# Optimization experiments

Hardware: AMD Instinct MI355X
Metric: run time of the kernel (lower is better)

## Reference

```python
import jax, jax.numpy as jnp
import numpy as np

D = 512          # embedding_dim (cfg.hidden_size)
K = 1024         # codebook_size
DECAY = 0.99
EPS = 1e-05
COMMITMENT_COST = 0.25


def setup_inputs() -> dict:
    key = jax.random.key(0)
    k1, k2, k3 = jax.random.split(key, 3)
    return {
        "inputs": jax.random.normal(k1, (32, 1024, D), dtype=jnp.float32),
        "embedding_weight": jax.random.normal(k2, (K, D), dtype=jnp.float32),
        "ema_cluster_size": jnp.zeros((K,), dtype=jnp.float32),
        "ema_w": jax.random.normal(k3, (K, D), dtype=jnp.float32),
    }


def reference(inputs, embedding_weight, ema_cluster_size, ema_w):
    input_shape = inputs.shape
    flat = inputs.reshape(-1, D)  # [N, D]

    # Squared L2 distances to every codebook entry: [N, K]
    distances = (
        jnp.sum(flat ** 2, axis=1, keepdims=True)
        + jnp.sum(embedding_weight ** 2, axis=1)
        - 2.0 * flat @ embedding_weight.T
    )
    idx = jnp.argmin(distances, axis=1)                      # [N]
    encodings = jax.nn.one_hot(idx, K, dtype=flat.dtype)     # [N, K]

    # ---- EMA codebook update (training path) ----
    counts = jnp.sum(encodings, axis=0)                      # == bincount(idx)
    new_cs = ema_cluster_size * DECAY + (1.0 - DECAY) * counts
    n = jnp.sum(new_cs)
    new_cs = (new_cs + EPS) / (n + K * EPS) * n              # Laplace smoothing
    # dw = encodings.T @ flat, done as a fused gather-reduce instead of dense matmul
    dw = jax.ops.segment_sum(flat, idx, num_segments=K)      # [K, D]
    new_ema_w = ema_w * DECAY + (1.0 - DECAY) * dw
    new_embedding = new_ema_w / new_cs[:, None]              # updated codebook

    # quantized = encodings @ new_embedding, expressed as a gather
    quantized = new_embedding[idx].reshape(input_shape)

    e_latent_loss = jnp.mean((jax.lax.stop_gradient(quantized) - inputs) ** 2)
    loss = COMMITMENT_COST * e_latent_loss

    # straight-through estimator
    quantized = inputs + jax.lax.stop_gradient(quantized - inputs)

    avg_probs = jnp.mean(encodings, axis=0)
    perplexity = jnp.exp(-jnp.sum(avg_probs * jnp.log(avg_probs + 1e-10)))
    return (loss, quantized, perplexity, encodings)
```

## Files before the change

### kernel.cpp

```cpp
#include <hip/hip_runtime.h>

#define NROWS 32768
#define DIM   512
#define KC    1024

typedef __attribute__((ext_vector_type(8)))  short short8v;
typedef __attribute__((ext_vector_type(16))) float f32x16;

__global__ __launch_bounds__(256) void k_enorm(const float* __restrict__ E,
                                               float* __restrict__ en2) {
    int w = threadIdx.x >> 6, lane = threadIdx.x & 63;
    int c = blockIdx.x * 4 + w;
    const float* row = E + (size_t)c * DIM;
    float4 a = *reinterpret_cast<const float4*>(&row[lane * 8]);
    float4 b = *reinterpret_cast<const float4*>(&row[lane * 8 + 4]);
    float s = a.x*a.x + a.y*a.y + a.z*a.z + a.w*a.w
            + b.x*b.x + b.y*b.y + b.z*b.z + b.w*b.w;
    #pragma unroll
    for (int off = 32; off; off >>= 1) s += __shfl_xor(s, off);
    if (!lane) en2[c] = s;
}

__device__ __forceinline__ void split_bf16(float v, short& hi, short& lo) {
    unsigned u = __float_as_uint(v);
    unsigned r = u + 0x7FFFu + ((u >> 16) & 1u);
    hi = (short)(r >> 16);
    float hif = __uint_as_float(r & 0xFFFF0000u);
    float rem = v - hif;
    unsigned u2 = __float_as_uint(rem);
    unsigned r2 = u2 + 0x7FFFu + ((u2 >> 16) & 1u);
    lo = (short)(r2 >> 16);
}

__device__ __forceinline__ unsigned long long pack_key(float d, int c) {
    unsigned u = __float_as_uint(d);
    u = (u & 0x80000000u) ? ~u : (u | 0x80000000u);
    return ((unsigned long long)u << 32) | (unsigned)c;
}

__global__ __launch_bounds__(256, 2) void k_argmin(const float* __restrict__ x,
                                                   const float* __restrict__ E,
                                                   const float* __restrict__ en2,
                                                   unsigned long long* __restrict__ packed) {
    __shared__ short xhi[128][48], xlo[128][48];
    __shared__ short ehi[128][48], elo[128][48];
    const int tid = threadIdx.x;
    const int w = tid >> 6, l = tid & 63;
    const int wr = w >> 1, wc = w & 1;
    const int l31 = l & 31, lh = l >> 5;

    int bid = blockIdx.x;
    int xcd = bid & 7, j = bid >> 3;
    int row0 = (xcd * 32 + (j >> 3)) * 128;
    int c0   = (j & 7) * 128;

    f32x16 acc[2][2];
    #pragma unroll
    for (int a = 0; a < 2; ++a)
        #pragma unroll
        for (int b = 0; b < 2; ++b)
            #pragma unroll
            for (int r = 0; r < 16; ++r) acc[a][b][r] = 0.f;

    float4 rx[4], re[4];
    #pragma unroll
    for (int h = 0; h < 4; ++h) {
        int s = tid + h * 256, r = s >> 3, f4 = s & 7;
        rx[h] = *reinterpret_cast<const float4*>(&x[(size_t)(row0 + r) * DIM + f4 * 4]);
        re[h] = *reinterpret_cast<const float4*>(&E[(size_t)(c0   + r) * DIM + f4 * 4]);
    }

    for (int dt = 0; dt < DIM; dt += 32) {
        __syncthreads();
        #pragma unroll
        for (int h = 0; h < 4; ++h) {
            int s = tid + h * 256, r = s >> 3, f4 = s & 7;
            short4 h4, l4;
            split_bf16(rx[h].x, h4.x, l4.x); split_bf16(rx[h].y, h4.y, l4.y);
            split_bf16(rx[h].z, h4.z, l4.z); split_bf16(rx[h].w, h4.w, l4.w);
            *reinterpret_cast<short4*>(&xhi[r][f4 * 4]) = h4;
            *reinterpret_cast<short4*>(&xlo[r][f4 * 4]) = l4;
            split_bf16(re[h].x, h4.x, l4.x); split_bf16(re[h].y, h4.y, l4.y);
            split_bf16(re[h].z, h4.z, l4.z); split_bf16(re[h].w, h4.w, l4.w);
            *reinterpret_cast<short4*>(&ehi[r][f4 * 4]) = h4;
            *reinterpret_cast<short4*>(&elo[r][f4 * 4]) = l4;
        }
        __syncthreads();
        if (dt + 32 < DIM) {
            #pragma unroll
            for (int h = 0; h < 4; ++h) {
                int s = tid + h * 256, r = s >> 3, f4 = s & 7;
                rx[h] = *reinterpret_cast<const float4*>(
                    &x[(size_t)(row0 + r) * DIM + dt + 32 + f4 * 4]);
                re[h] = *reinterpret_cast<const float4*>(
                    &E[(size_t)(c0   + r) * DIM + dt + 32 + f4 * 4]);
            }
        }
        #pragma unroll
        for (int ks = 0; ks < 2; ++ks) {
            const int kb = ks * 16 + lh * 8;
            short8v axh[2], axl[2], beh[2], bel[2];
            #pragma unroll
            for (int tm = 0; tm < 2; ++tm) {
                int row = wr * 64 + tm * 32 + l31;
                axh[tm] = *reinterpret_cast<const short8v*>(&xhi[row][kb]);
                axl[tm] = *reinterpret_cast<const short8v*>(&xlo[row][kb]);
            }
            #pragma unroll
            for (int tn = 0; tn < 2; ++tn) {
                int col = wc * 64 + tn * 32 + l31;
                beh[tn] = *reinterpret_cast<const short8v*>(&ehi[col][kb]);
                bel[tn] = *reinterpret_cast<const short8v*>(&elo[col][kb]);
            }
            #pragma unroll
            for (int tm = 0; tm < 2; ++tm)
                #pragma unroll
                for (int tn = 0; tn < 2; ++tn) {
                    acc[tm][tn] = __builtin_amdgcn_mfma_f32_32x32x16_bf16(
                        axh[tm], beh[tn], acc[tm][tn], 0, 0, 0);
                    acc[tm][tn] = __builtin_amdgcn_mfma_f32_32x32x16_bf16(
                        axh[tm], bel[tn], acc[tm][tn], 0, 0, 0);
                    acc[tm][tn] = __builtin_amdgcn_mfma_f32_32x32x16_bf16(
                        axl[tm], beh[tn], acc[tm][tn], 0, 0, 0);
                }
        }
    }

    float e2[2];
    #pragma unroll
    for (int tn = 0; tn < 2; ++tn) e2[tn] = en2[c0 + wc * 64 + tn * 32 + l31];
    const int cA = c0 + wc * 64 + l31;
    #pragma unroll
    for (int tm = 0; tm < 2; ++tm) {
        #pragma unroll
        for (int r = 0; r < 16; ++r) {
            float d0 = fmaf(-2.f, acc[tm][0][r], e2[0]);
            float d1 = fmaf(-2.f, acc[tm][1][r], e2[1]);
            unsigned long long k0 = pack_key(d0, cA);
            unsigned long long k1 = pack_key(d1, cA + 32);
            unsigned long long key = k0 < k1 ? k0 : k1;
            #pragma unroll
            for (int off = 1; off < 32; off <<= 1) {
                unsigned long long o = __shfl_xor(key, off);
                if (o < key) key = o;
            }
            if (l31 == 0) {
                int grow = row0 + wr * 64 + tm * 32 + (r & 3) + 8 * (r >> 2) + 4 * lh;
                atomicMin(&packed[grow], key);
            }
        }
    }
}

__global__ __launch_bounds__(256) void k_hist(const unsigned long long* __restrict__ packed,
                                              int* __restrict__ idx,
                                              int* __restrict__ counts) {
    __shared__ int h[KC];
    for (int i = threadIdx.x; i < KC; i += 256) h[i] = 0;
    __syncthreads();
    int g = blockIdx.x * 256 + threadIdx.x;
    int c = (int)(unsigned)(packed[g] & 0xFFFFFFFFull);
    idx[g] = c;
    atomicAdd(&h[c], 1);
    __syncthreads();
    for (int i = threadIdx.x; i < KC; i += 256)
        if (h[i]) atomicAdd(&counts[i], h[i]);
}

__global__ __launch_bounds__(1024) void k_meta(const int* __restrict__ counts,
                                               const float* __restrict__ ema_cs,
                                               float* __restrict__ smoothed,
                                               int* __restrict__ offsets,
                                               int* __restrict__ cursor,
                                               float* __restrict__ perp_out) {
    __shared__ float red[KC];
    __shared__ int sc[KC];
    int t = threadIdx.x;
    int cnt = counts[t];
    float cs = ema_cs[t] * 0.99f + 0.01f * (float)cnt;
    red[t] = cs; __syncthreads();
    for (int s = 512; s; s >>= 1) { if (t < s) red[t] += red[t + s]; __syncthreads(); }
    float n = red[0];
    __syncthreads();
    float sm = (cs + 1e-5f) / (n + 1024.f * 1e-5f) * n;
    smoothed[t] = sm;
    float p = (float)cnt / 32768.f;
    red[t] = p * logf(p + 1e-10f);
    __syncthreads();
    for (int s = 512; s; s >>= 1) { if (t < s) red[t] += red[t + s]; __syncthreads(); }
    if (!t) perp_out[0] = expf(-red[0]);
    sc[t] = cnt; __syncthreads();
    for (int s = 1; s < KC; s <<= 1) {
        int v = (t >= s) ? sc[t - s] : 0;
        __syncthreads();
        sc[t] += v;
        __syncthreads();
    }
    int off = sc[t] - cnt;
    offsets[t] = off;
    cursor[t] = off;
}

__global__ __launch_bounds__(256) void k_scatter(const int* __restrict__ idx,
                                                 int* __restrict__ cursor,
                                                 int* __restrict__ bucket) {
    int g = blockIdx.x * 256 + threadIdx.x;
    int c = idx[g];
    int pos = atomicAdd(&cursor[c], 1);
    bucket[pos] = g;
}

__global__ __launch_bounds__(256) void k_enc(const int* __restrict__ idx,
                                             float* __restrict__ enc) {
    int t = threadIdx.x;
    int row = blockIdx.x * 8 + (t >> 5);
    int l32 = t & 31;
    int one = idx[row];
    float4* dst = reinterpret_cast<float4*>(enc + (size_t)row * KC);
    #pragma unroll
    for (int s = 0; s < 8; ++s) {
        int c4 = l32 + s * 32;
        int base = c4 * 4;
        float4 v;
        v.x = (one == base)     ? 1.f : 0.f;
        v.y = (one == base + 1) ? 1.f : 0.f;
        v.z = (one == base + 2) ? 1.f : 0.f;
        v.w = (one == base + 3) ? 1.f : 0.f;
        dst[c4] = v;
    }
}

__global__ __launch_bounds__(256) void k_dw(const float* __restrict__ x,
                                            const float* __restrict__ ema_w,
                                            const int* __restrict__ offsets,
                                            const int* __restrict__ counts,
                                            const int* __restrict__ bucket,
                                            const float* __restrict__ smoothed,
                                            float* __restrict__ newE) {
    __shared__ int rows[256];
    int k = blockIdx.x, t = threadIdx.x;
    int beg = offsets[k], m = counts[k];
    float a0 = 0.f, a1 = 0.f;
    for (int base = 0; base < m; base += 256) {
        int n = min(256, m - base);
        __syncthreads();
        if (t < n) rows[t] = bucket[beg + base + t];
        __syncthreads();
        int i = 0;
        for (; i + 4 <= n; i += 4) {
            int r0 = rows[i], r1 = rows[i + 1], r2 = rows[i + 2], r3 = rows[i + 3];
            float v00 = x[(size_t)r0 * DIM + t];
            float v01 = x[(size_t)r0 * DIM + t + 256];
            float v10 = x[(size_t)r1 * DIM + t];
            float v11 = x[(size_t)r1 * DIM + t + 256];
            float v20 = x[(size_t)r2 * DIM + t];
            float v21 = x[(size_t)r2 * DIM + t + 256];
            float v30 = x[(size_t)r3 * DIM + t];
            float v31 = x[(size_t)r3 * DIM + t + 256];
            a0 += v00 + v10 + v20 + v30;
            a1 += v01 + v11 + v21 + v31;
        }
        for (; i < n; ++i) {
            int r = rows[i];
            a0 += x[(size_t)r * DIM + t];
            a1 += x[(size_t)r * DIM + t + 256];
        }
    }
    float sm = smoothed[k];
    newE[(size_t)k * DIM + t]       = (ema_w[(size_t)k * DIM + t]       * 0.99f + 0.01f * a0) / sm;
    newE[(size_t)k * DIM + t + 256] = (ema_w[(size_t)k * DIM + t + 256] * 0.99f + 0.01f * a1) / sm;
}

__global__ __launch_bounds__(256) void k_quant(const float* __restrict__ x,
                                               const int* __restrict__ idx,
                                               const float* __restrict__ newE,
                                               float* __restrict__ outq,
                                               float* __restrict__ partials) {
    int t0 = blockIdx.x * 256 + threadIdx.x;
    float lp = 0.f;
    #pragma unroll 4
    for (int s = 0; s < 16; ++s) {
        int e = t0 + s * 1048576;
        int row = e >> 9;
        int c = idx[row];
        float in = x[e];
        float q = newE[(size_t)c * DIM + (e & 511)];
        float d = q - in;
        outq[e] = in + d;
        lp += d * d;
    }
    #pragma unroll
    for (int off = 32; off; off >>= 1) lp += __shfl_xor(lp, off);
    __shared__ float wr[4];
    int lane = threadIdx.x & 63, w = threadIdx.x >> 6;
    if (!lane) wr[w] = lp;
    __syncthreads();
    if (threadIdx.x == 0) partials[blockIdx.x] = wr[0] + wr[1] + wr[2] + wr[3];
}

__global__ __launch_bounds__(256) void k_lossfin(const float* __restrict__ partials,
                                                 float* __restrict__ out0) {
    __shared__ double red[256];
    double s = 0.0;
    for (int i = threadIdx.x; i < 4096; i += 256) s += (double)partials[i];
    red[threadIdx.x] = s; __syncthreads();
    for (int st = 128; st; st >>= 1) {
        if (threadIdx.x < st) red[threadIdx.x] += red[threadIdx.x + st];
        __syncthreads();
    }
    if (!threadIdx.x) out0[0] = (float)(0.25 * red[0] / 16777216.0);
}

extern "C" void kernel_launch(void* const* d_in, const int* in_sizes, int n_in,
                              void* d_out, int out_size, void* d_ws, size_t ws_size,
                              hipStream_t stream) {
    const float* x   = (const float*)d_in[0];
    const float* E   = (const float*)d_in[1];
    const float* ecs = (const float*)d_in[2];
    const float* emw = (const float*)d_in[3];
    float* out = (float*)d_out;

    char* ws = (char*)d_ws;
    int*   idx      = (int*)(ws + 0);
    int*   bucket   = (int*)(ws + 131072);
    float* en2      = (float*)(ws + 262144);
    int*   counts   = (int*)(ws + 266240);
    int*   offsets  = (int*)(ws + 270336);
    int*   cursor   = (int*)(ws + 274432);
    float* smoothed = (float*)(ws + 278528);
    float* newE     = (float*)(ws + 282624);
    float* partials = (float*)(ws + 282624 + 2097152);
    unsigned long long* packed = (unsigned long long*)newE;

    float* out_loss = out;
    float* out_q    = out + 1;
    float* out_perp = out + 16777217;
    float* out_enc  = out + 16777218;

    hipMemsetAsync(counts, 0, KC * sizeof(int), stream);
    hipMemsetAsync(packed, 0xFF, NROWS * sizeof(unsigned long long), stream);

    k_enorm  <<<KC / 4, 256, 0, stream>>>(E, en2);
    k_argmin <<<(NROWS / 128) * 8, 256, 0, stream>>>(x, E, en2, packed);
    k_hist   <<<NROWS / 256, 256, 0, stream>>>(packed, idx, counts);
    k_meta   <<<1, 1024, 0, stream>>>(counts, ecs, smoothed, offsets, cursor, out_perp);
    k_scatter<<<NROWS / 256, 256, 0, stream>>>(idx, cursor, bucket);
    k_enc    <<<NROWS / 8, 256, 0, stream>>>(idx, out_enc);
    k_dw     <<<KC, 256, 0, stream>>>(x, emw, offsets, counts, bucket, smoothed, newE);
    k_quant  <<<4096, 256, 0, stream>>>(x, idx, newE, out_q, partials);
    k_lossfin<<<1, 256, 0, stream>>>(partials, out_loss);
}
```

Baseline: 346.7 us.

## Pre-split inputs into MFMA-fragment bf16 layout and load directly from global

Adds a pre-pass kernel that splits x and E into bf16 hi/lo parts once and stores them in a layout matching the MFMA register fragments, reusing the encodings output buffer as scratch. The argmin GEMM then loads fragments straight from global memory with no LDS staging, no barriers and no repeated split work, and raises the occupancy hint to 3 blocks. This removes split recomputation (each x tile was re-split for 8 column blocks) and the LDS round trip. In exchange it adds an extra pass writing about 64MB of fragment data and reading it back, and the global loads are not cooperatively shared across waves.

```diff
diff --git a/kernel.cpp b/kernel.cpp
--- a/kernel.cpp
+++ b/kernel.cpp
@@ -38,12 +38,49 @@
     return ((unsigned long long)u << 32) | (unsigned)c;
 }
 
-__global__ __launch_bounds__(256, 2) void k_argmin(const float* __restrict__ x,
-                                                   const float* __restrict__ E,
+__global__ __launch_bounds__(256) void k_split(const float* __restrict__ x,
+                                               const float* __restrict__ E,
+                                               short* __restrict__ xfrag,
+                                               short* __restrict__ efrag) {
+    __shared__ short hbuf[32][520];
+    __shared__ short lbuf[32][520];
+    int b = blockIdx.x, t = threadIdx.x;
+    const float* src;
+    short* dst;
+    if (b < NROWS / 32) {
+        src = x + (size_t)b * 32 * DIM;
+        dst = xfrag + (size_t)b * 32768;
+    } else {
+        src = E + (size_t)(b - NROWS / 32) * 32 * DIM;
+        dst = efrag + (size_t)(b - NROWS / 32) * 32768;
+    }
+    #pragma unroll
+    for (int f = 0; f < 16; ++f) {
+        int u = t + f * 256;
+        int row = u >> 7, c4 = (u & 127) * 4;
+        float4 v = *reinterpret_cast<const float4*>(&src[row * DIM + c4]);
+        short4 h4, l4;
+        split_bf16(v.x, h4.x, l4.x); split_bf16(v.y, h4.y, l4.y);
+        split_bf16(v.z, h4.z, l4.z); split_bf16(v.w, h4.w, l4.w);
+        *reinterpret_cast<short4*>(&hbuf[row][c4]) = h4;
+        *reinterpret_cast<short4*>(&lbuf[row][c4]) = l4;
+    }
+    __syncthreads();
+    #pragma unroll
+    for (int f = 0; f < 16; ++f) {
+        int u = t + f * 256;
+        int lane = u & 63, h = (u >> 6) & 1, kb = u >> 7;
+        int row = lane & 31, k0 = kb * 16 + (lane >> 5) * 8;
+        const short* s = h ? &lbuf[row][k0] : &hbuf[row][k0];
+        short8v val = *reinterpret_cast<const short8v*>(s);
+        *reinterpret_cast<short8v*>(&dst[(size_t)u * 8]) = val;
+    }
+}
+
+__global__ __launch_bounds__(256, 3) void k_argmin(const short* __restrict__ xfrag,
+                                                   const short* __restrict__ efrag,
                                                    const float* __restrict__ en2,
                                                    unsigned long long* __restrict__ packed) {
-    __shared__ short xhi[128][48], xlo[128][48];
-    __shared__ short ehi[128][48], elo[128][48];
     const int tid = threadIdx.x;
     const int w = tid >> 6, l = tid & 63;
     const int wr = w >> 1, wc = w & 1;
@@ -54,6 +91,15 @@
     int row0 = (xcd * 32 + (j >> 3)) * 128;
     int c0   = (j & 7) * 128;
 
+    const short* ab[2];
+    const short* bb[2];
+    #pragma unroll
+    for (int tm = 0; tm < 2; ++tm)
+        ab[tm] = xfrag + (size_t)(row0 / 32 + wr * 2 + tm) * 32768 + l * 8;
+    #pragma unroll
+    for (int tn = 0; tn < 2; ++tn)
+        bb[tn] = efrag + (size_t)(c0 / 32 + wc * 2 + tn) * 32768 + l * 8;
+
     f32x16 acc[2][2];
     #pragma unroll
     for (int a = 0; a < 2; ++a)
@@ -62,68 +108,30 @@
             #pragma unroll
             for (int r = 0; r < 16; ++r) acc[a][b][r] = 0.f;
 
-    float4 rx[4], re[4];
-    #pragma unroll
-    for (int h = 0; h < 4; ++h) {
-        int s = tid + h * 256, r = s >> 3, f4 = s & 7;
-        rx[h] = *reinterpret_cast<const float4*>(&x[(size_t)(row0 + r) * DIM + f4 * 4]);
-        re[h] = *reinterpret_cast<const float4*>(&E[(size_t)(c0   + r) * DIM + f4 * 4]);
-    }
-
-    for (int dt = 0; dt < DIM; dt += 32) {
-        __syncthreads();
-        #pragma unroll
-        for (int h = 0; h < 4; ++h) {
-            int s = tid + h * 256, r = s >> 3, f4 = s & 7;
-            short4 h4, l4;
-            split_bf16(rx[h].x, h4.x, l4.x); split_bf16(rx[h].y, h4.y, l4.y);
-            split_bf16(rx[h].z, h4.z, l4.z); split_bf16(rx[h].w, h4.w, l4.w);
-            *reinterpret_cast<short4*>(&xhi[r][f4 * 4]) = h4;
-            *reinterpret_cast<short4*>(&xlo[r][f4 * 4]) = l4;
-            split_bf16(re[h].x, h4.x, l4.x); split_bf16(re[h].y, h4.y, l4.y);
-            split_bf16(re[h].z, h4.z, l4.z); split_bf16(re[h].w, h4.w, l4.w);
-            *reinterpret_cast<short4*>(&ehi[r][f4 * 4]) = h4;
-            *reinterpret_cast<short4*>(&elo[r][f4 * 4]) = l4;
-        }
-        __syncthreads();
-        if (dt + 32 < DIM) {
-            #pragma unroll
-            for (int h = 0; h < 4; ++h) {
-                int s = tid + h * 256, r = s >> 3, f4 = s & 7;
-                rx[h] = *reinterpret_cast<const float4*>(
-                    &x[(size_t)(row0 + r) * DIM + dt + 32 + f4 * 4]);
-                re[h] = *reinterpret_cast<const float4*>(
-                    &E[(size_t)(c0   + r) * DIM + dt + 32 + f4 * 4]);
-            }
-        }
-        #pragma unroll
-        for (int ks = 0; ks < 2; ++ks) {
-            const int kb = ks * 16 + lh * 8;
-            short8v axh[2], axl[2], beh[2], bel[2];
-            #pragma unroll
-            for (int tm = 0; tm < 2; ++tm) {
-                int row = wr * 64 + tm * 32 + l31;
-                axh[tm] = *reinterpret_cast<const short8v*>(&xhi[row][kb]);
-                axl[tm] = *reinterpret_cast<const short8v*>(&xlo[row][kb]);
-            }
+    #pragma unroll 2
+    for (int kb = 0; kb < 32; ++kb) {
+        short8v axh[2], axl[2], beh[2], bel[2];
+        #pragma unroll
+        for (int tm = 0; tm < 2; ++tm) {
+            axh[tm] = *reinterpret_cast<const short8v*>(ab[tm] + kb * 1024);
+            axl[tm] = *reinterpret_cast<const short8v*>(ab[tm] + kb * 1024 + 512);
+        }
+        #pragma unroll
+        for (int tn = 0; tn < 2; ++tn) {
+            beh[tn] = *reinterpret_cast<const short8v*>(bb[tn] + kb * 1024);
+            bel[tn] = *reinterpret_cast<const short8v*>(bb[tn] + kb * 1024 + 512);
+        }
+        #pragma unroll
+        for (int tm = 0; tm < 2; ++tm)
             #pragma unroll
             for (int tn = 0; tn < 2; ++tn) {
-                int col = wc * 64 + tn * 32 + l31;
-                beh[tn] = *reinterpret_cast<const short8v*>(&ehi[col][kb]);
-                bel[tn] = *reinterpret_cast<const short8v*>(&elo[col][kb]);
+                acc[tm][tn] = __builtin_amdgcn_mfma_f32_32x32x16_bf16(
+                    axh[tm], beh[tn], acc[tm][tn], 0, 0, 0);
+                acc[tm][tn] = __builtin_amdgcn_mfma_f32_32x32x16_bf16(
+                    axh[tm], bel[tn], acc[tm][tn], 0, 0, 0);
+                acc[tm][tn] = __builtin_amdgcn_mfma_f32_32x32x16_bf16(
+                    axl[tm], beh[tn], acc[tm][tn], 0, 0, 0);
             }
-            #pragma unroll
-            for (int tm = 0; tm < 2; ++tm)
-                #pragma unroll
-                for (int tn = 0; tn < 2; ++tn) {
-                    acc[tm][tn] = __builtin_amdgcn_mfma_f32_32x32x16_bf16(
-                        axh[tm], beh[tn], acc[tm][tn], 0, 0, 0);
-                    acc[tm][tn] = __builtin_amdgcn_mfma_f32_32x32x16_bf16(
-                        axh[tm], bel[tn], acc[tm][tn], 0, 0, 0);
-                    acc[tm][tn] = __builtin_amdgcn_mfma_f32_32x32x16_bf16(
-                        axl[tm], beh[tn], acc[tm][tn], 0, 0, 0);
-                }
-        }
     }
 
     float e2[2];
@@ -337,11 +345,15 @@
     float* out_perp = out + 16777217;
     float* out_enc  = out + 16777218;
 
+    short* xfrag = (short*)out_enc;
+    short* efrag = xfrag + (size_t)NROWS * DIM * 2;
+
     hipMemsetAsync(counts, 0, KC * sizeof(int), stream);
     hipMemsetAsync(packed, 0xFF, NROWS * sizeof(unsigned long long), stream);
 
     k_enorm  <<<KC / 4, 256, 0, stream>>>(E, en2);
-    k_argmin <<<(NROWS / 128) * 8, 256, 0, stream>>>(x, E, en2, packed);
+    k_split  <<<NROWS / 32 + KC / 32, 256, 0, stream>>>(x, E, xfrag, efrag);
+    k_argmin <<<(NROWS / 128) * 8, 256, 0, stream>>>(xfrag, efrag, en2, packed);
     k_hist   <<<NROWS / 256, 256, 0, stream>>>(packed, idx, counts);
     k_meta   <<<1, 1024, 0, stream>>>(counts, ecs, smoothed, offsets, cursor, out_perp);
     k_scatter<<<NROWS / 256, 256, 0, stream>>>(idx, cursor, bucket);
```

Result: no change. 340.7 us (-1.7%).
